# Performance work log

Measured on AMD Instinct MI355X. Metric: run time of the kernel, lower is better.

Reference implementation:

```python
import jax, jax.numpy as jnp
import numpy as np

N_NODES = 100000
E2 = 1600000
E3 = 1600000
ES = 100000
HID = 64


def _mlp_3x3(x_in, W1, b1, W2, b2):
    # x_in: [E, d_in] -> mobility [E, 3, 3]
    h = jax.nn.relu(x_in @ W1 + b1)
    out = h @ W2 + b2  # [E, 9]
    return out.reshape(-1, 3, 3)


def setup_inputs() -> dict:
    key = jax.random.key(0)
    ks = jax.random.split(key, 20)
    inp = {}
    inp["x"] = jax.random.normal(ks[0], (N_NODES, 3), dtype=jnp.float32)
    inp["edge_2body"] = jax.random.randint(ks[1], (2, E2), 0, N_NODES)
    inp["edge_3body"] = jax.random.randint(ks[2], (3, E3), 0, N_NODES)
    inp["edge_2bodySelf"] = jax.random.randint(ks[3], (2, ES), 0, N_NODES)
    inp["edge_1body"] = jax.random.randint(ks[4], (2, ES), 0, N_NODES)
    inp["edge_attr_2body"] = jax.random.normal(ks[5], (E2, 3), dtype=jnp.float32)
    inp["edge_attr_3body"] = jax.random.normal(ks[6], (E3, 3), dtype=jnp.float32)
    inp["edge_attr_2bodySelf"] = jax.random.normal(ks[7], (ES, 3), dtype=jnp.float32)
    inp["edge_attr_1body"] = jax.random.normal(ks[8], (ES, 3), dtype=jnp.float32)
    s = 0.1
    # nn_2body: 3 -> HID -> 9
    inp["W1_2b"] = jax.random.normal(ks[9], (3, HID), dtype=jnp.float32) * s
    inp["b1_2b"] = jnp.zeros((HID,), jnp.float32)
    inp["W2_2b"] = jax.random.normal(ks[10], (HID, 9), dtype=jnp.float32) * s
    inp["b2_2b"] = jnp.zeros((9,), jnp.float32)
    # nn_3body: 6 -> HID -> 9
    inp["W1_3b"] = jax.random.normal(ks[11], (6, HID), dtype=jnp.float32) * s
    inp["b1_3b"] = jnp.zeros((HID,), jnp.float32)
    inp["W2_3b"] = jax.random.normal(ks[12], (HID, 9), dtype=jnp.float32) * s
    inp["b2_3b"] = jnp.zeros((9,), jnp.float32)
    # nn_self: 3 -> HID -> 9
    inp["W1_s"] = jax.random.normal(ks[13], (3, HID), dtype=jnp.float32) * s
    inp["b1_s"] = jnp.zeros((HID,), jnp.float32)
    inp["W2_s"] = jax.random.normal(ks[14], (HID, 9), dtype=jnp.float32) * s
    inp["b2_s"] = jnp.zeros((9,), jnp.float32)
    return inp


def reference(x, edge_2body, edge_3body, edge_2bodySelf, edge_1body,
              edge_attr_2body, edge_attr_3body, edge_attr_2bodySelf, edge_attr_1body,
              W1_2b, b1_2b, W2_2b, b2_2b,
              W1_3b, b1_3b, W2_3b, b2_3b,
              W1_s, b1_s, W2_s, b2_s):
    n = x.shape[0]
    # ---- 2-body: gather -> MLP -> per-edge 3x3 matvec -> scatter-add ----
    d2 = x[edge_2body[0]] - x[edge_2body[1]]  # xj - xi, [E2,3]
    mob2 = _mlp_3x3(d2, W1_2b, b1_2b, W2_2b, b2_2b)
    y2 = jnp.einsum('eij,ej->ei', mob2, edge_attr_2body)
    v2 = jax.ops.segment_sum(y2, edge_2body[1], num_segments=n)
    # ---- 3-body ----
    xj = x[edge_3body[0]]
    xk = x[edge_3body[1]]
    xi = x[edge_3body[2]]
    d3 = jnp.concatenate((xk - xj, xi - xk), axis=1)  # [E3,6]
    mob3 = _mlp_3x3(d3, W1_3b, b1_3b, W2_3b, b2_3b)
    y3 = jnp.einsum('eij,ej->ei', mob3, edge_attr_3body)
    v3 = jax.ops.segment_sum(y3, edge_3body[2], num_segments=n)
    # ---- 2-body self ----
    ds = x[edge_2bodySelf[0]] - x[edge_2bodySelf[1]]
    mobs = _mlp_3x3(ds, W1_s, b1_s, W2_s, b2_s)
    ys = jnp.einsum('eij,ej->ei', mobs, edge_attr_2bodySelf)
    vs = jax.ops.segment_sum(ys, edge_2bodySelf[1], num_segments=n)
    # edge_1body / edge_attr_1body unused in original forward
    return v2 + v3 + vs
```

## Files before the change

kernel.cpp:

```cpp
#include <hip/hip_runtime.h>


constexpr int HIDDEN = 64;
constexpr int NB_MAX = 256;
constexpr int NPB_SHIFT = 9;
constexpr int NPB = 1 << NPB_SHIFT;
constexpr int TILE_F = NPB * 3;
constexpr int NET_SLOT = 1024;
constexpr int NET_USED = 640;

typedef _Float16 h2_t __attribute__((ext_vector_type(2)));

__device__ __forceinline__ unsigned packh2(float a, float b) {
    auto h = __builtin_amdgcn_cvt_pkrtz(a, b);
    return __builtin_bit_cast(unsigned, h);
}
__device__ __forceinline__ float fdot2u(unsigned a, unsigned b, float c) {
    h2_t ha = __builtin_bit_cast(h2_t, a);
    h2_t hb = __builtin_bit_cast(h2_t, b);
#if __has_builtin(__builtin_amdgcn_fdot2)
    return __builtin_amdgcn_fdot2(ha, hb, c, false);
#else
    return fmaf((float)ha.x, (float)hb.x, fmaf((float)ha.y, (float)hb.y, c));
#endif
}


__global__ __launch_bounds__(256) void setup_kernel(
    const float* __restrict__ x, int n_nodes, float4* __restrict__ x4,
    int* __restrict__ gcount,
    const float* __restrict__ W1_2b, const float* __restrict__ b1_2b,
    const float* __restrict__ W2_2b, const float* __restrict__ b2_2b,
    const float* __restrict__ W1_s,  const float* __restrict__ b1_s,
    const float* __restrict__ W2_s,  const float* __restrict__ b2_s,
    const float* __restrict__ W1_3b, const float* __restrict__ b1_3b,
    const float* __restrict__ W2_3b, const float* __restrict__ b2_3b,
    unsigned* __restrict__ nets)
{
    const int blk = blockIdx.x;
    const int tid = threadIdx.x;
    if (blk < 3) {
        const float *W1, *b1, *W2, *b2; int din;
        if (blk == 0) { W1 = W1_2b; b1 = b1_2b; W2 = W2_2b; b2 = b2_2b; din = 3; }
        else if (blk == 1) { W1 = W1_s; b1 = b1_s; W2 = W2_s; b2 = b2_s; din = 3; }
        else { W1 = W1_3b; b1 = b1_3b; W2 = W2_3b; b2 = b2_3b; din = 6; }
        unsigned* slot = nets + blk * NET_SLOT;
        float* slotf = (float*)slot;
        if (tid < 64) {
            int hh = tid;
            if (din == 3) {
                slot[hh] = packh2(W1[0 * HIDDEN + hh], W1[1 * HIDDEN + hh]);
                slotf[560 + hh] = W1[2 * HIDDEN + hh];
            } else {
                #pragma unroll
                for (int r = 0; r < 3; ++r)
                    slot[hh * 3 + r] =
                        packh2(W1[(2 * r) * HIDDEN + hh], W1[(2 * r + 1) * HIDDEN + hh]);
            }
            slotf[192 + hh] = b1[hh];
        }
        for (int t = tid; t < 288; t += 256) {
            int hh2 = t / 9, i = t - hh2 * 9;
            slot[256 + t] = packh2(W2[(2 * hh2) * 9 + i], W2[(2 * hh2 + 1) * 9 + i]);
        }
        if (tid < 9) slotf[544 + tid] = b2[tid];
        if (blk == 0) gcount[tid] = 0;
    } else {
        int i = (blk - 3) * 256 + tid;
        if (i < n_nodes)
            x4[i] = make_float4(x[3 * i], x[3 * i + 1], x[3 * i + 2], 0.0f);
    }
}

__global__ __launch_bounds__(256) void p1_edge_kernel(
    const float4* __restrict__ x4,
    const int* __restrict__ e0, long long E0, const float* __restrict__ at0,
    const int* __restrict__ e1, long long E1, const float* __restrict__ at1,
    const int* __restrict__ e2, long long E2, const float* __restrict__ at2,
    int g0, int g1,
    const unsigned* __restrict__ nets,
    float4* __restrict__ records, int* __restrict__ gcount, int cap)
{
    constexpr int BLK = 256;
    constexpr int KPT = 4;

    __shared__ int s_hist[NB_MAX];
    __shared__ int s_base[NB_MAX];
    __shared__ int s_rank[NB_MAX];
    __shared__ unsigned s_net[NET_USED];

    const int blk = blockIdx.x;
    const int* edges; long long E; const float* attr;
    int bidx, nblk, din3;
    const unsigned* wp;
    if (blk < g0)           { edges = e0; E = E0; attr = at0; bidx = blk;          nblk = g0;                 din3 = 1; wp = nets; }
    else if (blk < g0 + g1) { edges = e1; E = E1; attr = at1; bidx = blk - g0;     nblk = g1;                 din3 = 1; wp = nets + NET_SLOT; }
    else                    { edges = e2; E = E2; attr = at2; bidx = blk - g0 - g1; nblk = gridDim.x - g0 - g1; din3 = 0; wp = nets + 2 * NET_SLOT; }

    const int tid = threadIdx.x;
    long long span = (E + nblk - 1) / nblk;
    span = (span + 1023) & ~1023LL;
    const long long lo = (long long)bidx * span;
    const long long hi = (lo + span < E) ? (lo + span) : E;
    if (lo >= E) return;

    const bool e_aligned = ((E & 3) == 0);

    for (int i = tid; i < NB_MAX; i += BLK) { s_hist[i] = 0; s_rank[i] = 0; }
    for (int i = tid; i < NET_USED; i += BLK) s_net[i] = wp[i];
    __syncthreads();

    const unsigned* w = s_net;
    const float* wf = (const float*)s_net;

    const long long dstrow = din3 ? E : 2 * E;
    for (long long t0 = lo; t0 < hi; t0 += BLK * KPT) {
        const long long be = t0 + (long long)tid * KPT;
        if (be >= hi) continue;
        if (e_aligned && be + KPT <= hi) {
            int4 r = *(const int4*)(edges + dstrow + be);
            atomicAdd(&s_hist[r.x >> NPB_SHIFT], 1);
            atomicAdd(&s_hist[r.y >> NPB_SHIFT], 1);
            atomicAdd(&s_hist[r.z >> NPB_SHIFT], 1);
            atomicAdd(&s_hist[r.w >> NPB_SHIFT], 1);
        } else {
            #pragma unroll
            for (int u = 0; u < KPT; ++u) {
                long long e = be + u;
                if (e < hi)
                    atomicAdd(&s_hist[edges[dstrow + e] >> NPB_SHIFT], 1);
            }
        }
    }
    __syncthreads();

    for (int i = tid; i < NB_MAX; i += BLK) {
        int h = s_hist[i];
        s_base[i] = (h > 0) ? atomicAdd(&gcount[i], h) : 0;
    }
    __syncthreads();

    for (long long t0 = lo; t0 < hi; t0 += BLK * KPT) {
        const long long be = t0 + (long long)tid * KPT;

        unsigned dp[KPT][3];
        float    d2s[KPT];
        float    a[KPT][3];
        int      dst[KPT];
        bool     valid[KPT];
        int      i0[KPT], i1[KPT], i2[KPT];

        const bool full = e_aligned && (be + KPT <= hi);
        if (full) {
            int4 r0 = *(const int4*)(edges + be);
            int4 r1 = *(const int4*)(edges + E + be);
            i0[0] = r0.x; i0[1] = r0.y; i0[2] = r0.z; i0[3] = r0.w;
            i1[0] = r1.x; i1[1] = r1.y; i1[2] = r1.z; i1[3] = r1.w;
            if (!din3) {
                int4 r2 = *(const int4*)(edges + 2 * E + be);
                i2[0] = r2.x; i2[1] = r2.y; i2[2] = r2.z; i2[3] = r2.w;
            }
            float4 a0 = *(const float4*)(attr + 3 * be);
            float4 a1 = *(const float4*)(attr + 3 * be + 4);
            float4 a2 = *(const float4*)(attr + 3 * be + 8);
            a[0][0] = a0.x; a[0][1] = a0.y; a[0][2] = a0.z;
            a[1][0] = a0.w; a[1][1] = a1.x; a[1][2] = a1.y;
            a[2][0] = a1.z; a[2][1] = a1.w; a[2][2] = a2.x;
            a[3][0] = a2.y; a[3][1] = a2.z; a[3][2] = a2.w;
            #pragma unroll
            for (int u = 0; u < KPT; ++u) valid[u] = true;
        } else {
            #pragma unroll
            for (int u = 0; u < KPT; ++u) {
                long long e = be + u;
                valid[u] = (e < hi);
                long long ee = valid[u] ? e : lo;
                i0[u] = edges[ee];
                i1[u] = edges[E + ee];
                if (!din3) i2[u] = edges[2 * E + ee];
                #pragma unroll
                for (int c = 0; c < 3; ++c) a[u][c] = attr[3 * ee + c];
            }
        }

        if (be >= hi) continue;

        #pragma unroll
        for (int u = 0; u < KPT; ++u) {
            if (din3) {
                dst[u] = i1[u];
                float4 xs = x4[i0[u]];
                float4 xt = x4[i1[u]];
                dp[u][0] = packh2(xs.x - xt.x, xs.y - xt.y);
                d2s[u]   = xs.z - xt.z;
                dp[u][1] = 0; dp[u][2] = 0;
            } else {
                dst[u] = i2[u];
                float4 xj = x4[i0[u]];
                float4 xk = x4[i1[u]];
                float4 xi = x4[i2[u]];
                dp[u][0] = packh2(xk.x - xj.x, xk.y - xj.y);
                dp[u][1] = packh2(xk.z - xj.z, xi.x - xk.x);
                dp[u][2] = packh2(xi.y - xk.y, xi.z - xk.z);
                d2s[u] = 0.f;
            }
        }

        float acc[KPT][9];
        #pragma unroll
        for (int u = 0; u < KPT; ++u)
            #pragma unroll
            for (int i = 0; i < 9; ++i) acc[u][i] = wf[544 + i];

        if (din3) {
            #pragma unroll 2
            for (int hh2 = 0; hh2 < HIDDEN / 2; ++hh2) {
                const unsigned wA = w[2 * hh2];
                const unsigned wB = w[2 * hh2 + 1];
                const float wcA = wf[560 + 2 * hh2];
                const float wcB = wf[561 + 2 * hh2];
                const float bbA = wf[192 + 2 * hh2];
                const float bbB = wf[193 + 2 * hh2];
                unsigned w2p[9];
                #pragma unroll
                for (int i = 0; i < 9; ++i) w2p[i] = w[256 + hh2 * 9 + i];
                #pragma unroll
                for (int u = 0; u < KPT; ++u) {
                    float preA = fmaf(d2s[u], wcA, fdot2u(dp[u][0], wA, bbA));
                    float preB = fmaf(d2s[u], wcB, fdot2u(dp[u][0], wB, bbB));
                    unsigned h2 = packh2(fmaxf(preA, 0.f), fmaxf(preB, 0.f));
                    #pragma unroll
                    for (int i = 0; i < 9; ++i)
                        acc[u][i] = fdot2u(h2, w2p[i], acc[u][i]);
                }
            }
        } else {
            #pragma unroll 2
            for (int hh2 = 0; hh2 < HIDDEN / 2; ++hh2) {
                const unsigned wA0 = w[(2 * hh2) * 3 + 0];
                const unsigned wA1 = w[(2 * hh2) * 3 + 1];
                const unsigned wA2 = w[(2 * hh2) * 3 + 2];
                const unsigned wB0 = w[(2 * hh2 + 1) * 3 + 0];
                const unsigned wB1 = w[(2 * hh2 + 1) * 3 + 1];
                const unsigned wB2 = w[(2 * hh2 + 1) * 3 + 2];
                const float bbA = wf[192 + 2 * hh2];
                const float bbB = wf[193 + 2 * hh2];
                unsigned w2p[9];
                #pragma unroll
                for (int i = 0; i < 9; ++i) w2p[i] = w[256 + hh2 * 9 + i];
                #pragma unroll
                for (int u = 0; u < KPT; ++u) {
                    float preA = fdot2u(dp[u][2], wA2,
                                 fdot2u(dp[u][1], wA1,
                                 fdot2u(dp[u][0], wA0, bbA)));
                    float preB = fdot2u(dp[u][2], wB2,
                                 fdot2u(dp[u][1], wB1,
                                 fdot2u(dp[u][0], wB0, bbB)));
                    unsigned h2 = packh2(fmaxf(preA, 0.f), fmaxf(preB, 0.f));
                    #pragma unroll
                    for (int i = 0; i < 9; ++i)
                        acc[u][i] = fdot2u(h2, w2p[i], acc[u][i]);
                }
            }
        }

        #pragma unroll
        for (int u = 0; u < KPT; ++u) {
            if (!valid[u]) continue;
            float y0 = fmaf(acc[u][0], a[u][0], fmaf(acc[u][1], a[u][1], acc[u][2] * a[u][2]));
            float y1 = fmaf(acc[u][3], a[u][0], fmaf(acc[u][4], a[u][1], acc[u][5] * a[u][2]));
            float y2 = fmaf(acc[u][6], a[u][0], fmaf(acc[u][7], a[u][1], acc[u][8] * a[u][2]));
            int b = dst[u] >> NPB_SHIFT;
            int r = atomicAdd(&s_rank[b], 1);
            int slot = s_base[b] + r;
            if (slot < cap)
                records[(size_t)b * cap + slot] =
                    make_float4(y0, y1, y2, __int_as_float(dst[u]));
        }
    }
}

__global__ __launch_bounds__(1024) void p2_bucket(
    const float4* __restrict__ records, const int* __restrict__ gcount,
    int cap, int n_nodes, float* __restrict__ out)
{
    __shared__ float s_acc[TILE_F];
    const int b = blockIdx.x;
    const int tid = threadIdx.x;

    for (int i = tid; i < TILE_F; i += 1024) s_acc[i] = 0.0f;
    __syncthreads();

    int cnt = gcount[b];
    if (cnt > cap) cnt = cap;
    const float4* rb = records + (size_t)b * cap;
    for (int i = tid; i < cnt; i += 1024) {
        float4 r = rb[i];
        int loc = __float_as_int(r.w) - (b << NPB_SHIFT);
        atomicAdd(&s_acc[loc * 3 + 0], r.x);
        atomicAdd(&s_acc[loc * 3 + 1], r.y);
        atomicAdd(&s_acc[loc * 3 + 2], r.z);
    }
    __syncthreads();

    const int start = (b << NPB_SHIFT) * 3;
    const int end = min(n_nodes * 3, ((b + 1) << NPB_SHIFT) * 3);
    for (int i = start + tid; i < end; i += 1024)
        out[i] = s_acc[i - start];
}

template <int DIN, int KPT>
__global__ __launch_bounds__(256) void edge_mlp_atomic(
    const float* __restrict__ x,
    const int* __restrict__ edges, long long E,
    const float* __restrict__ attr,
    const float* __restrict__ W1, const float* __restrict__ b1,
    const float* __restrict__ W2, const float* __restrict__ b2,
    float* __restrict__ out)
{
    const int tid = threadIdx.x;
    const long long base = (long long)blockIdx.x * (blockDim.x * KPT) + tid;
    float d[KPT][DIN]; float a[KPT][3]; int dst[KPT]; bool valid[KPT];
    #pragma unroll
    for (int u = 0; u < KPT; ++u) {
        long long e = base + (long long)u * blockDim.x;
        valid[u] = (e < E);
        long long ee = valid[u] ? e : 0;
        if constexpr (DIN == 3) {
            int s = edges[ee]; int t = edges[E + ee]; dst[u] = t;
            #pragma unroll
            for (int c = 0; c < 3; ++c)
                d[u][c] = x[3 * (long long)s + c] - x[3 * (long long)t + c];
        } else {
            int j = edges[ee]; int k = edges[E + ee]; int i = edges[2 * E + ee];
            dst[u] = i;
            #pragma unroll
            for (int c = 0; c < 3; ++c) {
                float xj = x[3 * (long long)j + c];
                float xk = x[3 * (long long)k + c];
                float xi = x[3 * (long long)i + c];
                d[u][c] = xk - xj; d[u][3 + c] = xi - xk;
            }
        }
        #pragma unroll
        for (int c = 0; c < 3; ++c) a[u][c] = attr[3 * ee + c];
    }
    float acc[KPT][9];
    #pragma unroll
    for (int u = 0; u < KPT; ++u)
        #pragma unroll
        for (int i = 0; i < 9; ++i) acc[u][i] = b2[i];
    #pragma unroll 4
    for (int hh = 0; hh < HIDDEN; ++hh) {
        const float bb = b1[hh];
        float w1r[DIN];
        #pragma unroll
        for (int r = 0; r < DIN; ++r) w1r[r] = W1[r * HIDDEN + hh];
        float w2r[9];
        #pragma unroll
        for (int i = 0; i < 9; ++i) w2r[i] = W2[hh * 9 + i];
        #pragma unroll
        for (int u = 0; u < KPT; ++u) {
            float pre = bb;
            #pragma unroll
            for (int r = 0; r < DIN; ++r) pre = fmaf(d[u][r], w1r[r], pre);
            const float h = fmaxf(pre, 0.0f);
            #pragma unroll
            for (int i = 0; i < 9; ++i) acc[u][i] = fmaf(h, w2r[i], acc[u][i]);
        }
    }
    #pragma unroll
    for (int u = 0; u < KPT; ++u) {
        if (!valid[u]) continue;
        float* o = out + 3 * (long long)dst[u];
        #pragma unroll
        for (int i = 0; i < 3; ++i) {
            float y = fmaf(acc[u][3 * i + 0], a[u][0],
                      fmaf(acc[u][3 * i + 1], a[u][1],
                           acc[u][3 * i + 2] * a[u][2]));
            atomicAdd(&o[i], y);
        }
    }
}

extern "C" void kernel_launch(void* const* d_in, const int* in_sizes, int n_in,
                              void* d_out, int out_size, void* d_ws, size_t ws_size,
                              hipStream_t stream)
{
    const float* x  = (const float*)d_in[0];
    const int*   e2 = (const int*)d_in[1];
    const int*   e3 = (const int*)d_in[2];
    const int*   es = (const int*)d_in[3];
    const float* a2 = (const float*)d_in[5];
    const float* a3 = (const float*)d_in[6];
    const float* as = (const float*)d_in[7];
    const float* W1_2b = (const float*)d_in[9];
    const float* b1_2b = (const float*)d_in[10];
    const float* W2_2b = (const float*)d_in[11];
    const float* b2_2b = (const float*)d_in[12];
    const float* W1_3b = (const float*)d_in[13];
    const float* b1_3b = (const float*)d_in[14];
    const float* W2_3b = (const float*)d_in[15];
    const float* b2_3b = (const float*)d_in[16];
    const float* W1_s  = (const float*)d_in[17];
    const float* b1_s  = (const float*)d_in[18];
    const float* W2_s  = (const float*)d_in[19];
    const float* b2_s  = (const float*)d_in[20];

    const long long E2 = in_sizes[1] / 2;
    const long long E3 = in_sizes[2] / 3;
    const long long ES = in_sizes[3] / 2;
    const long long Etot = E2 + E3 + ES;
    const int n_nodes = out_size / 3;
    const int nbuckets = (n_nodes + NPB - 1) >> NPB_SHIFT;

    float* out = (float*)d_out;

    const size_t off_nets = 1024;
    const size_t off_x4 = off_nets + 3 * NET_SLOT * 4;
    const size_t x4_bytes = (size_t)n_nodes * sizeof(float4);
    const size_t off_rec = (off_x4 + x4_bytes + 255) & ~(size_t)255;

    long long mean_per_bucket = (Etot + nbuckets - 1) / nbuckets;
    long long min_cap = mean_per_bucket + 1600;
    long long cap_avail =
        ((long long)ws_size - (long long)off_rec) / ((long long)nbuckets * 16);

    constexpr int SPAN = 2048;
    int g0 = (int)((E2 + SPAN - 1) / SPAN);
    int g1 = (int)((ES + SPAN - 1) / SPAN);
    int g2g = (int)((E3 + SPAN - 1) / SPAN);

    if (nbuckets <= NB_MAX && cap_avail >= min_cap) {
        long long capL = min_cap + 4096;
        if (capL > cap_avail) capL = cap_avail;
        int cap = (int)capL;
        int* gcount = (int*)d_ws;
        unsigned* nets = (unsigned*)((char*)d_ws + off_nets);
        float4* x4 = (float4*)((char*)d_ws + off_x4);
        float4* records = (float4*)((char*)d_ws + off_rec);

        int nb_pad = (n_nodes + 255) / 256;
        setup_kernel<<<3 + nb_pad, 256, 0, stream>>>(
            x, n_nodes, x4, gcount,
            W1_2b, b1_2b, W2_2b, b2_2b,
            W1_s,  b1_s,  W2_s,  b2_s,
            W1_3b, b1_3b, W2_3b, b2_3b,
            nets);

        p1_edge_kernel<<<g0 + g1 + g2g, 256, 0, stream>>>(
            x4,
            e2, E2, a2,
            es, ES, as,
            e3, E3, a3,
            g0, g1,
            nets, records, gcount, cap);

        p2_bucket<<<nbuckets, 1024, 0, stream>>>(records, gcount, cap, n_nodes, out);
    } else {
        hipMemsetAsync(out, 0, (size_t)out_size * sizeof(float), stream);
        constexpr int BLK = 256, KPT = 4;
        const long long per_blk = (long long)BLK * KPT;
        int a2g = (int)((E2 + per_blk - 1) / per_blk);
        int a3g = (int)((E3 + per_blk - 1) / per_blk);
        int asg = (int)((ES + per_blk - 1) / per_blk);
        if (a2g > 0)
            edge_mlp_atomic<3, KPT><<<a2g, BLK, 0, stream>>>(
                x, e2, E2, a2, W1_2b, b1_2b, W2_2b, b2_2b, out);
        if (a3g > 0)
            edge_mlp_atomic<6, KPT><<<a3g, BLK, 0, stream>>>(
                x, e3, E3, a3, W1_3b, b1_3b, W2_3b, b2_3b, out);
        if (asg > 0)
            edge_mlp_atomic<3, KPT><<<asg, BLK, 0, stream>>>(
                x, es, ES, as, W1_s, b1_s, W2_s, b2_s, out);
    }
}
```

Measured before the change: 313.1 us.

## Pack MLP weights per hidden pair, read via uniform loads, interleave block types

Repacks each network's weights into per-hidden-pair rows: W1, b1 and W2 for that pair are contiguous, and b2 sits at a fixed offset. The edge kernel now reads weights directly from global memory with block-uniform, vectorised loads (which the compiler may turn into scalar loads) instead of staging them in LDS. It also interleaves 2-body and 3-body blocks across the grid to balance their differing costs. The global atomic that reserves bin bases is no longer followed by its own barrier; the bases are published to shared memory after the first compute tile, so the atomic latency overlaps with compute. The trade-off is that weight fetches depend on cache hits rather than LDS, and a barrier now sits inside the main loop.

```diff
diff --git a/kernel.cpp b/kernel.cpp
--- a/kernel.cpp
+++ b/kernel.cpp
@@ -6,8 +6,7 @@
 constexpr int NPB_SHIFT = 9;
 constexpr int NPB = 1 << NPB_SHIFT;
 constexpr int TILE_F = NPB * 3;
-constexpr int NET_SLOT = 1024;
-constexpr int NET_USED = 640;
+constexpr int NET_SLOT = 1040;
 
 typedef _Float16 h2_t __attribute__((ext_vector_type(2)));
 
@@ -46,24 +45,36 @@
         else { W1 = W1_3b; b1 = b1_3b; W2 = W2_3b; b2 = b2_3b; din = 6; }
         unsigned* slot = nets + blk * NET_SLOT;
         float* slotf = (float*)slot;
-        if (tid < 64) {
-            int hh = tid;
+        if (tid < 32) {
+            const int h2 = tid, hA = 2 * h2, hB = 2 * h2 + 1;
             if (din == 3) {
-                slot[hh] = packh2(W1[0 * HIDDEN + hh], W1[1 * HIDDEN + hh]);
-                slotf[560 + hh] = W1[2 * HIDDEN + hh];
+                unsigned* row = slot + h2 * 16;
+                float* rowf = (float*)row;
+                row[0] = packh2(W1[0 * HIDDEN + hA], W1[1 * HIDDEN + hA]);
+                row[1] = packh2(W1[0 * HIDDEN + hB], W1[1 * HIDDEN + hB]);
+                rowf[2] = b1[hA]; rowf[3] = b1[hB];
+                rowf[4] = W1[2 * HIDDEN + hA]; rowf[5] = W1[2 * HIDDEN + hB];
+                #pragma unroll
+                for (int i = 0; i < 9; ++i)
+                    row[6 + i] = packh2(W2[hA * 9 + i], W2[hB * 9 + i]);
+                row[15] = 0;
             } else {
-                #pragma unroll
-                for (int r = 0; r < 3; ++r)
-                    slot[hh * 3 + r] =
-                        packh2(W1[(2 * r) * HIDDEN + hh], W1[(2 * r + 1) * HIDDEN + hh]);
-            }
-            slotf[192 + hh] = b1[hh];
-        }
-        for (int t = tid; t < 288; t += 256) {
-            int hh2 = t / 9, i = t - hh2 * 9;
-            slot[256 + t] = packh2(W2[(2 * hh2) * 9 + i], W2[(2 * hh2 + 1) * 9 + i]);
-        }
-        if (tid < 9) slotf[544 + tid] = b2[tid];
+                unsigned* row = slot + h2 * 32;
+                float* rowf = (float*)row;
+                #pragma unroll
+                for (int r = 0; r < 3; ++r) {
+                    row[r]     = packh2(W1[(2 * r) * HIDDEN + hA], W1[(2 * r + 1) * HIDDEN + hA]);
+                    row[3 + r] = packh2(W1[(2 * r) * HIDDEN + hB], W1[(2 * r + 1) * HIDDEN + hB]);
+                }
+                rowf[6] = b1[hA]; rowf[7] = b1[hB];
+                #pragma unroll
+                for (int i = 0; i < 9; ++i)
+                    row[8 + i] = packh2(W2[hA * 9 + i], W2[hB * 9 + i]);
+                #pragma unroll
+                for (int i = 17; i < 20; ++i) row[i] = 0;
+            }
+        }
+        if (tid >= 32 && tid < 41) slotf[1024 + (tid - 32)] = b2[tid - 32];
         if (blk == 0) gcount[tid] = 0;
     } else {
         int i = (blk - 3) * 256 + tid;
@@ -83,19 +94,32 @@
 {
     constexpr int BLK = 256;
     constexpr int KPT = 4;
+    static_assert(NB_MAX == BLK, "one reserve bin per thread");
 
     __shared__ int s_hist[NB_MAX];
     __shared__ int s_base[NB_MAX];
     __shared__ int s_rank[NB_MAX];
-    __shared__ unsigned s_net[NET_USED];
-
-    const int blk = blockIdx.x;
+
+    const int gA = g0 + g1;
+    const int gB = (int)gridDim.x - gA;
+    const int mn = (gA < gB) ? gA : gB;
+    int aidx = -1, b6 = -1;
+    {
+        const int idx = blockIdx.x;
+        if (idx < 2 * mn) { if (idx & 1) b6 = idx >> 1; else aidx = idx >> 1; }
+        else {
+            const int r = idx - 2 * mn;
+            if (gA > gB) aidx = mn + r; else b6 = mn + r;
+        }
+    }
+
     const int* edges; long long E; const float* attr;
     int bidx, nblk, din3;
     const unsigned* wp;
-    if (blk < g0)           { edges = e0; E = E0; attr = at0; bidx = blk;          nblk = g0;                 din3 = 1; wp = nets; }
-    else if (blk < g0 + g1) { edges = e1; E = E1; attr = at1; bidx = blk - g0;     nblk = g1;                 din3 = 1; wp = nets + NET_SLOT; }
-    else                    { edges = e2; E = E2; attr = at2; bidx = blk - g0 - g1; nblk = gridDim.x - g0 - g1; din3 = 0; wp = nets + 2 * NET_SLOT; }
+    if (aidx >= 0) {
+        if (aidx < g0) { edges = e0; E = E0; attr = at0; bidx = aidx;      nblk = g0; din3 = 1; wp = nets; }
+        else           { edges = e1; E = E1; attr = at1; bidx = aidx - g0; nblk = g1; din3 = 1; wp = nets + NET_SLOT; }
+    } else             { edges = e2; E = E2; attr = at2; bidx = b6;        nblk = gB; din3 = 0; wp = nets + 2 * NET_SLOT; }
 
     const int tid = threadIdx.x;
     long long span = (E + nblk - 1) / nblk;
@@ -106,12 +130,13 @@
 
     const bool e_aligned = ((E & 3) == 0);
 
+    const float* b2f = (const float*)(wp + 1024);
+    float b2r[9];
+    #pragma unroll
+    for (int i = 0; i < 9; ++i) b2r[i] = b2f[i];
+
     for (int i = tid; i < NB_MAX; i += BLK) { s_hist[i] = 0; s_rank[i] = 0; }
-    for (int i = tid; i < NET_USED; i += BLK) s_net[i] = wp[i];
     __syncthreads();
-
-    const unsigned* w = s_net;
-    const float* wf = (const float*)s_net;
 
     const long long dstrow = din3 ? E : 2 * E;
     for (long long t0 = lo; t0 < hi; t0 += BLK * KPT) {
@@ -134,12 +159,13 @@
     }
     __syncthreads();
 
-    for (int i = tid; i < NB_MAX; i += BLK) {
-        int h = s_hist[i];
-        s_base[i] = (h > 0) ? atomicAdd(&gcount[i], h) : 0;
-    }
-    __syncthreads();
-
+    int my_base = 0;
+    {
+        const int h = s_hist[tid];
+        if (h > 0) my_base = atomicAdd(&gcount[tid], h);
+    }
+
+    bool first = true;
     for (long long t0 = lo; t0 < hi; t0 += BLK * KPT) {
         const long long be = t0 + (long long)tid * KPT;
 
@@ -182,8 +208,6 @@
                 for (int c = 0; c < 3; ++c) a[u][c] = attr[3 * ee + c];
             }
         }
-
-        if (be >= hi) continue;
 
         #pragma unroll
         for (int u = 0; u < KPT; ++u) {
@@ -210,20 +234,21 @@
         #pragma unroll
         for (int u = 0; u < KPT; ++u)
             #pragma unroll
-            for (int i = 0; i < 9; ++i) acc[u][i] = wf[544 + i];
+            for (int i = 0; i < 9; ++i) acc[u][i] = b2r[i];
 
         if (din3) {
             #pragma unroll 2
             for (int hh2 = 0; hh2 < HIDDEN / 2; ++hh2) {
-                const unsigned wA = w[2 * hh2];
-                const unsigned wB = w[2 * hh2 + 1];
-                const float wcA = wf[560 + 2 * hh2];
-                const float wcB = wf[561 + 2 * hh2];
-                const float bbA = wf[192 + 2 * hh2];
-                const float bbB = wf[193 + 2 * hh2];
-                unsigned w2p[9];
-                #pragma unroll
-                for (int i = 0; i < 9; ++i) w2p[i] = w[256 + hh2 * 9 + i];
+                const uint4* rq = (const uint4*)(wp + (hh2 << 4));
+                const uint4 q0 = rq[0], q1 = rq[1], q2 = rq[2], q3 = rq[3];
+                const unsigned wA = q0.x;
+                const unsigned wB = q0.y;
+                const float bbA = __uint_as_float(q0.z);
+                const float bbB = __uint_as_float(q0.w);
+                const float wcA = __uint_as_float(q1.x);
+                const float wcB = __uint_as_float(q1.y);
+                const unsigned w2p[9] = {q1.z, q1.w, q2.x, q2.y, q2.z,
+                                         q2.w, q3.x, q3.y, q3.z};
                 #pragma unroll
                 for (int u = 0; u < KPT; ++u) {
                     float preA = fmaf(d2s[u], wcA, fdot2u(dp[u][0], wA, bbA));
@@ -237,17 +262,15 @@
         } else {
             #pragma unroll 2
             for (int hh2 = 0; hh2 < HIDDEN / 2; ++hh2) {
-                const unsigned wA0 = w[(2 * hh2) * 3 + 0];
-                const unsigned wA1 = w[(2 * hh2) * 3 + 1];
-                const unsigned wA2 = w[(2 * hh2) * 3 + 2];
-                const unsigned wB0 = w[(2 * hh2 + 1) * 3 + 0];
-                const unsigned wB1 = w[(2 * hh2 + 1) * 3 + 1];
-                const unsigned wB2 = w[(2 * hh2 + 1) * 3 + 2];
-                const float bbA = wf[192 + 2 * hh2];
-                const float bbB = wf[193 + 2 * hh2];
-                unsigned w2p[9];
-                #pragma unroll
-                for (int i = 0; i < 9; ++i) w2p[i] = w[256 + hh2 * 9 + i];
+                const uint4* rq = (const uint4*)(wp + (hh2 << 5));
+                const uint4 q0 = rq[0], q1 = rq[1], q2 = rq[2], q3 = rq[3];
+                const unsigned q4x = wp[(hh2 << 5) + 16];
+                const unsigned wA0 = q0.x, wA1 = q0.y, wA2 = q0.z;
+                const unsigned wB0 = q0.w, wB1 = q1.x, wB2 = q1.y;
+                const float bbA = __uint_as_float(q1.z);
+                const float bbB = __uint_as_float(q1.w);
+                const unsigned w2p[9] = {q2.x, q2.y, q2.z, q2.w, q3.x,
+                                         q3.y, q3.z, q3.w, q4x};
                 #pragma unroll
                 for (int u = 0; u < KPT; ++u) {
                     float preA = fdot2u(dp[u][2], wA2,
@@ -262,6 +285,12 @@
                         acc[u][i] = fdot2u(h2, w2p[i], acc[u][i]);
                 }
             }
+        }
+
+        if (first) {
+            s_base[tid] = my_base;
+            __syncthreads();
+            first = false;
         }
 
         #pragma unroll
```

New measurement: 334.6 us. 6.9% more time.
